# Kernel tuning notes

Measured on AMD Instinct MI355X. Metric: run time of the kernel, lower is better.

## Reference

```python
import jax, jax.numpy as jnp
import numpy as np

NEG_INF = -9e15  # same masking constant as the original
LEAKY_ALPHA = 0.2  # tf.nn.leaky_relu default


def setup_inputs() -> dict:
    key = jax.random.key(0)
    k1, k2, k3, k4 = jax.random.split(key, 4)
    N, D, F = 8192, 256, 64
    features = jax.random.normal(k1, (N, D), dtype=jnp.float32)
    adj = jax.random.randint(k2, (N, N), 0, 2, dtype=jnp.int32)
    W = jax.random.normal(k3, (D, F), dtype=jnp.float32) * (1.0 / np.sqrt(D))
    a = jax.random.normal(k4, (2 * F, 1), dtype=jnp.float32) * 0.1
    return {"features": features, "adj": adj, "W": W, "a": a}


def reference(features, adj, W, a):
    # h = X W : [N, F]
    h = features @ W
    F = h.shape[1]
    # a^T [h_i || h_j] = (h a1)_i + (h a2)_j  -- avoids the N*N*2F concat tensor
    a1, a2 = a[:F], a[F:]            # [F,1] each
    e = jax.nn.leaky_relu((h @ a1) + (h @ a2).T, LEAKY_ALPHA)  # [N, N]
    scores = jnp.where(adj > 0, e, jnp.float32(NEG_INF))
    attention = jax.nn.softmax(scores, axis=1)                  # masked softmax over neighbors j
    h_prime = attention @ h                                     # [N, F]
    return jax.nn.elu(h_prime)
```

## Files before the change

kernel.cpp:

```cpp
#include <hip/hip_runtime.h>
#include <hip/hip_bf16.h>
#include <math.h>

#define NN 8192
#define DD 256
#define FF 64
#define NSPLIT 8
#define JCHUNK (NN / NSPLIT)

typedef __attribute__((ext_vector_type(8))) short bf16x8;
typedef __attribute__((ext_vector_type(4))) float f32x4;

__device__ __forceinline__ float lrelu(float x) { return fmaxf(x, 0.2f * x); }
__device__ __forceinline__ short f2bf(float x) {
  union { __hip_bfloat16 b; short s; } u;
  u.b = __float2bfloat16(x);
  return u.s;
}

__global__ __launch_bounds__(256) void k_h(
    const float* __restrict__ feat, const float* __restrict__ W,
    const float* __restrict__ a, ushort* __restrict__ hT,
    float* __restrict__ s1, float* __restrict__ s2) {
  __shared__ __align__(16) ushort Wt[64 * 256];
  const int t = threadIdx.x;
#pragma unroll
  for (int it = 0; it < 16; ++it) {
    int e4 = (it * 256 + t) * 4;
    int k = e4 >> 6;
    int d = e4 & 63;
    float4 wv = *(const float4*)(W + e4);
    Wt[((d + 0) * 256 + k) ^ (((d + 0) & 7) << 3)] = (ushort)f2bf(wv.x);
    Wt[((d + 1) * 256 + k) ^ (((d + 1) & 7) << 3)] = (ushort)f2bf(wv.y);
    Wt[((d + 2) * 256 + k) ^ (((d + 2) & 7) << 3)] = (ushort)f2bf(wv.z);
    Wt[((d + 3) * 256 + k) ^ (((d + 3) & 7) << 3)] = (ushort)f2bf(wv.w);
  }
  __syncthreads();
  const int lane = t & 63, w = t >> 6;
  const int il = lane & 15, kg = lane >> 4;
  const int ibase = blockIdx.x * 64 + w * 16;
  const float* frow = feat + (size_t)(ibase + il) * DD + kg * 8;
  f32x4 acc[4] = {{0,0,0,0},{0,0,0,0},{0,0,0,0},{0,0,0,0}};
  for (int k0 = 0; k0 < DD; k0 += 32) {
    float4 fa = *(const float4*)(frow + k0);
    float4 fb = *(const float4*)(frow + k0 + 4);
    bf16x8 av;
    av[0] = f2bf(fa.x); av[1] = f2bf(fa.y); av[2] = f2bf(fa.z); av[3] = f2bf(fa.w);
    av[4] = f2bf(fb.x); av[5] = f2bf(fb.y); av[6] = f2bf(fb.z); av[7] = f2bf(fb.w);
#pragma unroll
    for (int f = 0; f < 4; ++f) {
      int d = f * 16 + il;
      int idx = (d * 256 + k0 + kg * 8) ^ ((d & 7) << 3);
      bf16x8 bv = *(const bf16x8*)(&Wt[idx]);
      acc[f] = __builtin_amdgcn_mfma_f32_16x16x32_bf16(av, bv, acc[f], 0, 0, 0);
    }
  }
  float a1v[4], a2v[4];
#pragma unroll
  for (int f = 0; f < 4; ++f) {
    a1v[f] = a[f * 16 + il];
    a2v[f] = a[FF + f * 16 + il];
  }
#pragma unroll
  for (int f = 0; f < 4; ++f) {
    int d = f * 16 + il;
    ushort4 hv;
    hv.x = (ushort)f2bf(acc[f][0]);
    hv.y = (ushort)f2bf(acc[f][1]);
    hv.z = (ushort)f2bf(acc[f][2]);
    hv.w = (ushort)f2bf(acc[f][3]);
    *(ushort4*)(hT + (size_t)d * NN + ibase + kg * 4) = hv;
  }
#pragma unroll
  for (int r = 0; r < 4; ++r) {
    float v1 = acc[0][r] * a1v[0] + acc[1][r] * a1v[1] +
               acc[2][r] * a1v[2] + acc[3][r] * a1v[3];
    float v2 = acc[0][r] * a2v[0] + acc[1][r] * a2v[1] +
               acc[2][r] * a2v[2] + acc[3][r] * a2v[3];
#pragma unroll
    for (int m = 1; m <= 8; m <<= 1) {
      v1 += __shfl_xor(v1, m);
      v2 += __shfl_xor(v2, m);
    }
    if (il == 0) {
      int i = ibase + kg * 4 + r;
      s1[i] = v1;
      s2[i] = v2;
    }
  }
}

__global__ __launch_bounds__(256) void k_attn(
    const int* __restrict__ adj, const ushort* __restrict__ hT,
    const float* __restrict__ s1g, const float* __restrict__ s2g,
    float* __restrict__ pacc, float* __restrict__ pl) {
  __shared__ float tr[4][16][65];
  const int t = threadIdx.x;
  const int lane = t & 63, w = t >> 6;
  const int il = lane & 15, kg = lane >> 4;
  const int ig = blockIdx.x >> 3, js = blockIdx.x & 7;
  const int ibase = ig * 64 + w * 16;
  const int i = ibase + il;
  const float s1v = s1g[i];
  const float mi = lrelu(s1v + 8.0f);
  float lacc = 0.f;
  f32x4 acc[4] = {{0,0,0,0},{0,0,0,0},{0,0,0,0},{0,0,0,0}};
  const size_t arow = (size_t)i * NN;
  const int jbase = js * JCHUNK + kg * 8;
#pragma unroll 2
  for (int jc = 0; jc < JCHUNK / 32; ++jc) {
    const int jl = jbase + jc * 32;
    const int4 av0 = *(const int4*)(adj + arow + jl);
    const int4 av1 = *(const int4*)(adj + arow + jl + 4);
    const float4 sa = *(const float4*)(s2g + jl);
    const float4 sb = *(const float4*)(s2g + jl + 4);
    float p0 = av0.x ? __expf(lrelu(s1v + sa.x) - mi) : 0.f;
    float p1 = av0.y ? __expf(lrelu(s1v + sa.y) - mi) : 0.f;
    float p2 = av0.z ? __expf(lrelu(s1v + sa.z) - mi) : 0.f;
    float p3 = av0.w ? __expf(lrelu(s1v + sa.w) - mi) : 0.f;
    float p4 = av1.x ? __expf(lrelu(s1v + sb.x) - mi) : 0.f;
    float p5 = av1.y ? __expf(lrelu(s1v + sb.y) - mi) : 0.f;
    float p6 = av1.z ? __expf(lrelu(s1v + sb.z) - mi) : 0.f;
    float p7 = av1.w ? __expf(lrelu(s1v + sb.w) - mi) : 0.f;
    lacc += ((p0 + p1) + (p2 + p3)) + ((p4 + p5) + (p6 + p7));
    bf16x8 pb;
    pb[0] = f2bf(p0); pb[1] = f2bf(p1); pb[2] = f2bf(p2); pb[3] = f2bf(p3);
    pb[4] = f2bf(p4); pb[5] = f2bf(p5); pb[6] = f2bf(p6); pb[7] = f2bf(p7);
#pragma unroll
    for (int f = 0; f < 4; ++f) {
      const bf16x8 hv = *(const bf16x8*)(hT + (size_t)(f * 16 + il) * NN + jl);
      acc[f] = __builtin_amdgcn_mfma_f32_16x16x32_bf16(hv, pb, acc[f], 0, 0, 0);
    }
  }
  lacc += __shfl_xor(lacc, 16);
  lacc += __shfl_xor(lacc, 32);
  if (lane < 16) pl[(size_t)js * NN + ibase + lane] = lacc;
#pragma unroll
  for (int f = 0; f < 4; ++f)
#pragma unroll
    for (int r = 0; r < 4; ++r) tr[w][il][f * 16 + kg * 4 + r] = acc[f][r];
#pragma unroll
  for (int r = 0; r < 16; ++r)
    pacc[((size_t)js * NN + ibase + r) * FF + lane] = tr[w][r][lane];
}

__global__ __launch_bounds__(256) void k_combine(
    const float* __restrict__ pacc, const float* __restrict__ pl,
    float* __restrict__ out) {
  const int idx = blockIdx.x * 256 + threadIdx.x;
  const int i = idx >> 6;
  float s = 0.f, L = 0.f;
#pragma unroll
  for (int sp = 0; sp < NSPLIT; ++sp) {
    s += pacc[(size_t)sp * NN * FF + idx];
    L += pl[(size_t)sp * NN + i];
  }
  float x = s / fmaxf(L, 1e-30f);
  out[idx] = x > 0.f ? x : expm1f(x);
}

extern "C" void kernel_launch(void* const* d_in, const int* in_sizes, int n_in,
                              void* d_out, int out_size, void* d_ws, size_t ws_size,
                              hipStream_t stream) {
  const float* feat = (const float*)d_in[0];
  const int* adj = (const int*)d_in[1];
  const float* W = (const float*)d_in[2];
  const float* a = (const float*)d_in[3];
  float* out = (float*)d_out;

  ushort* hT = (ushort*)d_ws;
  float* s1 = (float*)(hT + (size_t)FF * NN);
  float* s2 = s1 + NN;
  float* pl = s2 + NN;
  float* pacc = pl + (size_t)NSPLIT * NN;

  hipLaunchKernelGGL(k_h, dim3(NN / 64), dim3(256), 0, stream, feat, W, a, hT, s1, s2);
  hipLaunchKernelGGL(k_attn, dim3((NN / 64) * NSPLIT), dim3(256), 0, stream,
                     adj, hT, s1, s2, pacc, pl);
  hipLaunchKernelGGL(k_combine, dim3(NN * FF / 256), dim3(256), 0, stream,
                     pacc, pl, out);
}
```

Before: 420.8 us.

## Precompute bf16 W transpose, split k_h per-feature across waves, double j-splits

```diff
diff --git a/kernel.cpp b/kernel.cpp
--- a/kernel.cpp
+++ b/kernel.cpp
@@ -5,7 +5,7 @@
 #define NN 8192
 #define DD 256
 #define FF 64
-#define NSPLIT 8
+#define NSPLIT 16
 #define JCHUNK (NN / NSPLIT)
 
 typedef __attribute__((ext_vector_type(8))) short bf16x8;
@@ -18,75 +18,64 @@
   return u.s;
 }
 
+__global__ __launch_bounds__(256) void k_pre(const float* __restrict__ W,
+                                             ushort* __restrict__ WT) {
+  const int e4 = (blockIdx.x * 256 + threadIdx.x) * 4;
+  const float4 wv = *(const float4*)(W + e4);
+  const int k = e4 >> 6, d = e4 & 63;
+  WT[(d + 0) * DD + k] = (ushort)f2bf(wv.x);
+  WT[(d + 1) * DD + k] = (ushort)f2bf(wv.y);
+  WT[(d + 2) * DD + k] = (ushort)f2bf(wv.z);
+  WT[(d + 3) * DD + k] = (ushort)f2bf(wv.w);
+}
+
 __global__ __launch_bounds__(256) void k_h(
-    const float* __restrict__ feat, const float* __restrict__ W,
+    const float* __restrict__ feat, const ushort* __restrict__ WT,
     const float* __restrict__ a, ushort* __restrict__ hT,
     float* __restrict__ s1, float* __restrict__ s2) {
-  __shared__ __align__(16) ushort Wt[64 * 256];
-  const int t = threadIdx.x;
+  __shared__ float sp1[4][16], sp2[4][16];
+  const int t = threadIdx.x, lane = t & 63, w = t >> 6;
+  const int il = lane & 15, kg = lane >> 4;
+  const int ibase = blockIdx.x * 16;
+  const int d = w * 16 + il;
+  const float* frow = feat + (size_t)(ibase + il) * DD + kg * 8;
+  const ushort* wrow = WT + (size_t)d * DD + kg * 8;
+  f32x4 acc = {0.f, 0.f, 0.f, 0.f};
 #pragma unroll
-  for (int it = 0; it < 16; ++it) {
-    int e4 = (it * 256 + t) * 4;
-    int k = e4 >> 6;
-    int d = e4 & 63;
-    float4 wv = *(const float4*)(W + e4);
-    Wt[((d + 0) * 256 + k) ^ (((d + 0) & 7) << 3)] = (ushort)f2bf(wv.x);
-    Wt[((d + 1) * 256 + k) ^ (((d + 1) & 7) << 3)] = (ushort)f2bf(wv.y);
-    Wt[((d + 2) * 256 + k) ^ (((d + 2) & 7) << 3)] = (ushort)f2bf(wv.z);
-    Wt[((d + 3) * 256 + k) ^ (((d + 3) & 7) << 3)] = (ushort)f2bf(wv.w);
-  }
-  __syncthreads();
-  const int lane = t & 63, w = t >> 6;
-  const int il = lane & 15, kg = lane >> 4;
-  const int ibase = blockIdx.x * 64 + w * 16;
-  const float* frow = feat + (size_t)(ibase + il) * DD + kg * 8;
-  f32x4 acc[4] = {{0,0,0,0},{0,0,0,0},{0,0,0,0},{0,0,0,0}};
   for (int k0 = 0; k0 < DD; k0 += 32) {
-    float4 fa = *(const float4*)(frow + k0);
-    float4 fb = *(const float4*)(frow + k0 + 4);
+    const float4 fa = *(const float4*)(frow + k0);
+    const float4 fb = *(const float4*)(frow + k0 + 4);
     bf16x8 av;
     av[0] = f2bf(fa.x); av[1] = f2bf(fa.y); av[2] = f2bf(fa.z); av[3] = f2bf(fa.w);
     av[4] = f2bf(fb.x); av[5] = f2bf(fb.y); av[6] = f2bf(fb.z); av[7] = f2bf(fb.w);
-#pragma unroll
-    for (int f = 0; f < 4; ++f) {
-      int d = f * 16 + il;
-      int idx = (d * 256 + k0 + kg * 8) ^ ((d & 7) << 3);
-      bf16x8 bv = *(const bf16x8*)(&Wt[idx]);
-      acc[f] = __builtin_amdgcn_mfma_f32_16x16x32_bf16(av, bv, acc[f], 0, 0, 0);
-    }
+    const bf16x8 bv = *(const bf16x8*)(wrow + k0);
+    acc = __builtin_amdgcn_mfma_f32_16x16x32_bf16(av, bv, acc, 0, 0, 0);
   }
-  float a1v[4], a2v[4];
-#pragma unroll
-  for (int f = 0; f < 4; ++f) {
-    a1v[f] = a[f * 16 + il];
-    a2v[f] = a[FF + f * 16 + il];
-  }
-#pragma unroll
-  for (int f = 0; f < 4; ++f) {
-    int d = f * 16 + il;
-    ushort4 hv;
-    hv.x = (ushort)f2bf(acc[f][0]);
-    hv.y = (ushort)f2bf(acc[f][1]);
-    hv.z = (ushort)f2bf(acc[f][2]);
-    hv.w = (ushort)f2bf(acc[f][3]);
-    *(ushort4*)(hT + (size_t)d * NN + ibase + kg * 4) = hv;
-  }
+  ushort4 hv;
+  hv.x = (ushort)f2bf(acc[0]);
+  hv.y = (ushort)f2bf(acc[1]);
+  hv.z = (ushort)f2bf(acc[2]);
+  hv.w = (ushort)f2bf(acc[3]);
+  *(ushort4*)(hT + (size_t)d * NN + ibase + kg * 4) = hv;
+  const float a1v = a[d], a2v = a[FF + d];
 #pragma unroll
   for (int r = 0; r < 4; ++r) {
-    float v1 = acc[0][r] * a1v[0] + acc[1][r] * a1v[1] +
-               acc[2][r] * a1v[2] + acc[3][r] * a1v[3];
-    float v2 = acc[0][r] * a2v[0] + acc[1][r] * a2v[1] +
-               acc[2][r] * a2v[2] + acc[3][r] * a2v[3];
+    float v1 = acc[r] * a1v;
+    float v2 = acc[r] * a2v;
 #pragma unroll
     for (int m = 1; m <= 8; m <<= 1) {
       v1 += __shfl_xor(v1, m);
       v2 += __shfl_xor(v2, m);
     }
     if (il == 0) {
-      int i = ibase + kg * 4 + r;
-      s1[i] = v1;
-      s2[i] = v2;
+      sp1[w][kg * 4 + r] = v1;
+      sp2[w][kg * 4 + r] = v2;
     }
+  }
+  __syncthreads();
+  if (t < 16) {
+    s1[ibase + t] = sp1[0][t] + sp1[1][t] + sp1[2][t] + sp1[3][t];
+    s2[ibase + t] = sp2[0][t] + sp2[1][t] + sp2[2][t] + sp2[3][t];
   }
 }
 
@@ -98,7 +87,7 @@
   const int t = threadIdx.x;
   const int lane = t & 63, w = t >> 6;
   const int il = lane & 15, kg = lane >> 4;
-  const int ig = blockIdx.x >> 3, js = blockIdx.x & 7;
+  const int ig = blockIdx.x >> 4, js = blockIdx.x & 15;
   const int ibase = ig * 64 + w * 16;
   const int i = ibase + il;
   const float s1v = s1g[i];
@@ -107,7 +96,7 @@
   f32x4 acc[4] = {{0,0,0,0},{0,0,0,0},{0,0,0,0},{0,0,0,0}};
   const size_t arow = (size_t)i * NN;
   const int jbase = js * JCHUNK + kg * 8;
-#pragma unroll 2
+#pragma unroll 4
   for (int jc = 0; jc < JCHUNK / 32; ++jc) {
     const int jl = jbase + jc * 32;
     const int4 av0 = *(const int4*)(adj + arow + jl);
@@ -169,12 +158,14 @@
   float* out = (float*)d_out;
 
   ushort* hT = (ushort*)d_ws;
-  float* s1 = (float*)(hT + (size_t)FF * NN);
+  ushort* WT = hT + (size_t)FF * NN;
+  float* s1 = (float*)(WT + (size_t)FF * DD);
   float* s2 = s1 + NN;
   float* pl = s2 + NN;
   float* pacc = pl + (size_t)NSPLIT * NN;
 
-  hipLaunchKernelGGL(k_h, dim3(NN / 64), dim3(256), 0, stream, feat, W, a, hT, s1, s2);
+  hipLaunchKernelGGL(k_pre, dim3(DD * FF / 1024), dim3(256), 0, stream, W, WT);
+  hipLaunchKernelGGL(k_h, dim3(NN / 16), dim3(256), 0, stream, feat, WT, a, hT, s1, s2);
   hipLaunchKernelGGL(k_attn, dim3((NN / 64) * NSPLIT), dim3(256), 0, stream,
                      adj, hT, s1, s2, pacc, pl);
   hipLaunchKernelGGL(k_combine, dim3(NN * FF / 256), dim3(256), 0, stream,
```

Result: no change. 417.3 us (-0.8%).
